# Performance work log

Measured on AMD Instinct MI355X. Metric: run time of the kernel, lower is better.

The kernel has to match this reference:

```python
import jax, jax.numpy as jnp
import numpy as np
from jax import lax

WINDOW_SIZE = 11
SIGMA = 1.5
C1 = 0.01 ** 2
C2 = 0.03 ** 2


def _gaussian_window(channels: int) -> jnp.ndarray:
    x = np.arange(WINDOW_SIZE)
    g = np.exp(-((x - WINDOW_SIZE // 2) ** 2) / (2.0 * SIGMA ** 2))
    g = g / g.sum()
    w2d = np.outer(g, g).astype(np.float32)  # [k,k]
    # depthwise kernel: [C, 1, k, k] in OIHW with feature_group_count=C
    return jnp.asarray(np.tile(w2d[None, None], (channels, 1, 1, 1)))


def _depthwise_blur(x: jnp.ndarray, window: jnp.ndarray) -> jnp.ndarray:
    pad = WINDOW_SIZE // 2
    return lax.conv_general_dilated(
        x, window,
        window_strides=(1, 1),
        padding=[(pad, pad), (pad, pad)],
        feature_group_count=x.shape[1],
        dimension_numbers=("NCHW", "OIHW", "NCHW"),
    )


def setup_inputs() -> dict:
    key = jax.random.key(0)
    k1, k2 = jax.random.split(key)
    pred = jax.random.normal(k1, (16, 3, 512, 512), dtype=jnp.float32)
    target = jax.random.normal(k2, (16, 3, 512, 512), dtype=jnp.float32)
    return {"pred": pred, "target": target}


def reference(pred, target):
    pred = (pred + 1.0) / 2.0
    target = (target + 1.0) / 2.0
    channels = pred.shape[1]
    window = _gaussian_window(channels)

    mu_p = _depthwise_blur(pred, window)
    mu_t = _depthwise_blur(target, window)
    mu_p_sq = mu_p * mu_p
    mu_t_sq = mu_t * mu_t
    mu_pt = mu_p * mu_t

    sigma_p_sq = _depthwise_blur(pred * pred, window) - mu_p_sq
    sigma_t_sq = _depthwise_blur(target * target, window) - mu_t_sq
    sigma_pt = _depthwise_blur(pred * target, window) - mu_pt

    ssim_map = ((2.0 * mu_pt + C1) * (2.0 * sigma_pt + C2)) / (
        (mu_p_sq + mu_t_sq + C1) * (sigma_p_sq + sigma_t_sq + C2)
    )
    return 1.0 - jnp.mean(ssim_map)
```

## Files before the change

### kernel.cpp

```cpp
#include <hip/hip_runtime.h>
#include <math.h>


#define IMG 512
#define TW 64
#define TH 16
#define GXD 8
#define GYD 32
#define GZD 48
#define NB (GXD * GYD * GZD)
#define VBS 88
#define C1c 0.0001f
#define C2c 0.0009f
#define NTOTAL 12582912.0f

typedef short bf16x8 __attribute__((ext_vector_type(8)));
typedef float f32x4 __attribute__((ext_vector_type(4)));
typedef float f32x2 __attribute__((ext_vector_type(2)));

struct GaussB { unsigned short gb[11]; };

__device__ __forceinline__ unsigned int pkbf(float a, float b) {
    return __builtin_amdgcn_perm(__float_as_uint(b), __float_as_uint(a),
                                 0x07060302u);
}

template <bool USE_ATOMIC>
__global__ __launch_bounds__(320, 6) void ssim_main(
    const float* __restrict__ pred,
    const float* __restrict__ target,
    float* __restrict__ sink,
    GaussB gwb)
{
    __shared__ unsigned short Wmat[16][32];
    __shared__ unsigned short vb[5][16][VBS];
    __shared__ float red[5];

    const int tid  = threadIdx.x;
    const int w    = tid >> 6;
    const int lane = tid & 63;
    const int quad = lane >> 4;
    const int n16  = lane & 15;
    const int tx0  = blockIdx.x * TW;
    const int ty0  = blockIdx.y * TH;
    const float* __restrict__ pbase = pred   + (size_t)blockIdx.z * (IMG * IMG);
    const float* __restrict__ tbase = target + (size_t)blockIdx.z * (IMG * IMG);

    for (int idx = tid; idx < 512; idx += 320) {
        int i = idx >> 5, k = idx & 31, d = k - i;
        Wmat[i][k] = (d >= 0 && d <= 10) ? gwb.gb[d] : 0;
    }
    __syncthreads();
    const bf16x8 wfrag = *(const bf16x8*)&Wmat[n16][quad * 8];

    const int gx   = tx0 - 5 + 16 * w + n16;
    const bool xin = (unsigned)gx < (unsigned)IMG;
    const int k0   = quad * 8;
    const int gy0  = ty0 - 5 + k0;
    const int vcol = 16 * w + 4 * quad;
    const f32x4 z = {0.0f, 0.0f, 0.0f, 0.0f};

    float pv[8], tv[8];
    {
        const bool ok = xin & (gy0 >= 0) & (gy0 <= IMG - 8);
        if (ok) {
            const float* pp = pbase + gy0 * IMG + gx;
            const float* tp = tbase + gy0 * IMG + gx;
            #pragma unroll
            for (int j = 0; j < 8; ++j) {
                pv[j] = pp[j * IMG];
                tv[j] = tp[j * IMG];
            }
        } else {
            #pragma unroll
            for (int j = 0; j < 8; ++j) {
                int gy = gy0 + j;
                bool in = xin && ((unsigned)gy < (unsigned)IMG);
                int idx = in ? (gy * IMG + gx) : 0;
                float a = pbase[idx];
                float b = tbase[idx];
                pv[j] = in ? a : 0.0f;
                tv[j] = in ? b : 0.0f;
            }
        }
    }

    const f32x2 halfv = {0.5f, 0.5f};
    f32x2 p2[4], t2[4];
    #pragma unroll
    for (int h = 0; h < 4; ++h) {
        f32x2 pr = {pv[2*h], pv[2*h+1]};
        f32x2 tr = {tv[2*h], tv[2*h+1]};
        p2[h] = pr * halfv + halfv;
        t2[h] = tr * halfv + halfv;
    }
    #pragma unroll
    for (int ch = 0; ch < 5; ++ch) {
        union { bf16x8 v; unsigned int u[4]; } f;
        #pragma unroll
        for (int h = 0; h < 4; ++h) {
            f32x2 q;
            if      (ch == 0) q = p2[h];
            else if (ch == 1) q = t2[h];
            else if (ch == 2) q = p2[h] * p2[h];
            else if (ch == 3) q = t2[h] * t2[h];
            else              q = p2[h] * t2[h];
            f.u[h] = pkbf(q.x, q.y);
        }
        f32x4 d = __builtin_amdgcn_mfma_f32_16x16x32_bf16(f.v, wfrag, z, 0, 0, 0);
        union { ushort4 s; unsigned int u[2]; } pk;
        pk.u[0] = pkbf(d[0], d[1]);
        pk.u[1] = pkbf(d[2], d[3]);
        *(ushort4*)&vb[ch][n16][vcol] = pk.s;
    }
    __syncthreads();

    float lsum = 0.0f;
    if (w < 4) {
        f32x4 r[5];
        #pragma unroll
        for (int ch = 0; ch < 5; ++ch) {
            bf16x8 a = *(const bf16x8*)&vb[ch][n16][16 * w + 8 * quad];
            r[ch] = __builtin_amdgcn_mfma_f32_16x16x32_bf16(a, wfrag, z, 0, 0, 0);
        }
        const f32x2 twov = {2.0f, 2.0f};
        const f32x2 c1v  = {C1c, C1c};
        const f32x2 c2v  = {C2c, C2c};
        #pragma unroll
        for (int jj = 0; jj < 2; ++jj) {
            f32x2 mp  = {r[0][2*jj], r[0][2*jj+1]};
            f32x2 mt  = {r[1][2*jj], r[1][2*jj+1]};
            f32x2 epp = {r[2][2*jj], r[2][2*jj+1]};
            f32x2 ett = {r[3][2*jj], r[3][2*jj+1]};
            f32x2 ept = {r[4][2*jj], r[4][2*jj+1]};
            f32x2 mp2 = mp * mp;
            f32x2 mt2 = mt * mt;
            f32x2 mpt = mp * mt;
            f32x2 sp_ = epp - mp2;
            f32x2 st_ = ett - mt2;
            f32x2 spt = ept - mpt;
            f32x2 num = (mpt * twov + c1v) * (spt * twov + c2v);
            f32x2 den = (mp2 + mt2 + c1v) * (sp_ + st_ + c2v);
            lsum = fmaf(num.x, __builtin_amdgcn_rcpf(den.x), lsum);
            lsum = fmaf(num.y, __builtin_amdgcn_rcpf(den.y), lsum);
        }
    }

    #pragma unroll
    for (int off = 32; off > 0; off >>= 1)
        lsum += __shfl_down(lsum, off, 64);
    if (lane == 0) red[w] = lsum;
    __syncthreads();
    if (tid == 0) {
        float s = red[0] + red[1] + red[2] + red[3];
        if (USE_ATOMIC) {
            atomicAdd(sink, s);
        } else {
            int bid = blockIdx.x + GXD * (blockIdx.y + GYD * blockIdx.z);
            sink[bid] = s;
        }
    }
}

__global__ __launch_bounds__(256) void ssim_reduce(const float* __restrict__ partials,
                                                   float* __restrict__ out)
{
    __shared__ float red[4];
    const int tid = threadIdx.x;
    float s = 0.0f;
    const float4* p4 = (const float4*)partials;
    #pragma unroll
    for (int j = 0; j < NB / 1024; ++j) {
        float4 v = p4[tid + 256 * j];
        s += v.x + v.y + v.z + v.w;
    }
    #pragma unroll
    for (int off = 32; off > 0; off >>= 1)
        s += __shfl_down(s, off, 64);
    if ((tid & 63) == 0) red[tid >> 6] = s;
    __syncthreads();
    if (tid == 0)
        out[0] = 1.0f - (red[0] + red[1] + red[2] + red[3]) / NTOTAL;
}

__global__ void ssim_zero(float* accum) { accum[0] = 0.0f; }
__global__ void ssim_final(const float* accum, float* out) {
    out[0] = 1.0f - accum[0] / NTOTAL;
}

extern "C" void kernel_launch(void* const* d_in, const int* in_sizes, int n_in,
                              void* d_out, int out_size, void* d_ws, size_t ws_size,
                              hipStream_t stream) {
    const float* pred   = (const float*)d_in[0];
    const float* target = (const float*)d_in[1];
    float* out = (float*)d_out;

    GaussB gwb;
    double vals[11], s = 0.0;
    for (int i = 0; i < 11; ++i) {
        double d = (double)i - 5.0;
        vals[i] = exp(-(d * d) / (2.0 * 1.5 * 1.5));
        s += vals[i];
    }
    for (int i = 0; i < 11; ++i) {
        float f = (float)(vals[i] / s);
        unsigned int u;
        __builtin_memcpy(&u, &f, 4);
        unsigned int rounded = (u + 0x7FFFu + ((u >> 16) & 1u)) >> 16;
        gwb.gb[i] = (unsigned short)rounded;
    }

    dim3 grid(GXD, GYD, GZD);
    if (ws_size >= (size_t)NB * sizeof(float)) {
        float* partials = (float*)d_ws;
        ssim_main<false><<<grid, 320, 0, stream>>>(pred, target, partials, gwb);
        ssim_reduce<<<1, 256, 0, stream>>>(partials, out);
    } else {
        float* accum = (float*)d_ws;
        ssim_zero<<<1, 1, 0, stream>>>(accum);
        ssim_main<true><<<grid, 320, 0, stream>>>(pred, target, accum, gwb);
        ssim_final<<<1, 1, 0, stream>>>(accum, out);
    }
}
```

Measured before the change: 136.3 us.

## Process eight row tiles per block with double-buffered register prefetch

Each block now walks 8 vertical tiles instead of one, so the grid shrinks to 4 blocks in y. The next tile's global loads are issued into a second register set before the horizontal pass of the current tile, which hides load latency. It also spreads the Gaussian matrix setup and block launch cost over more work. In exchange there are fewer blocks (1536) to fill the GPU, more registers in use, and the 10-row halo is still reloaded for every tile. The reduce loop was generalised to handle the smaller partial count.

```diff
diff --git a/kernel.cpp b/kernel.cpp
--- a/kernel.cpp
+++ b/kernel.cpp
@@ -5,8 +5,9 @@
 #define IMG 512
 #define TW 64
 #define TH 16
+#define YPB 8
 #define GXD 8
-#define GYD 32
+#define GYD 4
 #define GZD 48
 #define NB (GXD * GYD * GZD)
 #define VBS 88
@@ -42,26 +43,22 @@
     const int quad = lane >> 4;
     const int n16  = lane & 15;
     const int tx0  = blockIdx.x * TW;
-    const int ty0  = blockIdx.y * TH;
+    const int tyb  = blockIdx.y * (TH * YPB);
     const float* __restrict__ pbase = pred   + (size_t)blockIdx.z * (IMG * IMG);
     const float* __restrict__ tbase = target + (size_t)blockIdx.z * (IMG * IMG);
-
-    for (int idx = tid; idx < 512; idx += 320) {
-        int i = idx >> 5, k = idx & 31, d = k - i;
-        Wmat[i][k] = (d >= 0 && d <= 10) ? gwb.gb[d] : 0;
-    }
-    __syncthreads();
-    const bf16x8 wfrag = *(const bf16x8*)&Wmat[n16][quad * 8];
 
     const int gx   = tx0 - 5 + 16 * w + n16;
     const bool xin = (unsigned)gx < (unsigned)IMG;
     const int k0   = quad * 8;
-    const int gy0  = ty0 - 5 + k0;
     const int vcol = 16 * w + 4 * quad;
     const f32x4 z = {0.0f, 0.0f, 0.0f, 0.0f};
 
-    float pv[8], tv[8];
-    {
+    float pvA[8], tvA[8], pvB[8], tvB[8];
+    float lsum = 0.0f;
+    bf16x8 wfrag;
+
+    auto load_tile = [&](int it, float (&pv)[8], float (&tv)[8]) {
+        const int gy0 = tyb + it * TH - 5 + k0;
         const bool ok = xin & (gy0 >= 0) & (gy0 <= IMG - 8);
         if (ok) {
             const float* pp = pbase + gy0 * IMG + gx;
@@ -83,67 +80,93 @@
                 tv[j] = in ? b : 0.0f;
             }
         }
-    }
-
-    const f32x2 halfv = {0.5f, 0.5f};
-    f32x2 p2[4], t2[4];
-    #pragma unroll
-    for (int h = 0; h < 4; ++h) {
-        f32x2 pr = {pv[2*h], pv[2*h+1]};
-        f32x2 tr = {tv[2*h], tv[2*h+1]};
-        p2[h] = pr * halfv + halfv;
-        t2[h] = tr * halfv + halfv;
-    }
-    #pragma unroll
-    for (int ch = 0; ch < 5; ++ch) {
-        union { bf16x8 v; unsigned int u[4]; } f;
+    };
+
+    load_tile(0, pvA, tvA);
+
+    for (int idx = tid; idx < 512; idx += 320) {
+        int i = idx >> 5, k = idx & 31, d = k - i;
+        Wmat[i][k] = (d >= 0 && d <= 10) ? gwb.gb[d] : 0;
+    }
+    __syncthreads();
+    wfrag = *(const bf16x8*)&Wmat[n16][quad * 8];
+
+    auto pass_v = [&](const float (&pv)[8], const float (&tv)[8]) {
+        const f32x2 halfv = {0.5f, 0.5f};
+        f32x2 p2[4], t2[4];
         #pragma unroll
         for (int h = 0; h < 4; ++h) {
-            f32x2 q;
-            if      (ch == 0) q = p2[h];
-            else if (ch == 1) q = t2[h];
-            else if (ch == 2) q = p2[h] * p2[h];
-            else if (ch == 3) q = t2[h] * t2[h];
-            else              q = p2[h] * t2[h];
-            f.u[h] = pkbf(q.x, q.y);
-        }
-        f32x4 d = __builtin_amdgcn_mfma_f32_16x16x32_bf16(f.v, wfrag, z, 0, 0, 0);
-        union { ushort4 s; unsigned int u[2]; } pk;
-        pk.u[0] = pkbf(d[0], d[1]);
-        pk.u[1] = pkbf(d[2], d[3]);
-        *(ushort4*)&vb[ch][n16][vcol] = pk.s;
-    }
-    __syncthreads();
-
-    float lsum = 0.0f;
-    if (w < 4) {
-        f32x4 r[5];
+            f32x2 pr = {pv[2*h], pv[2*h+1]};
+            f32x2 tr = {tv[2*h], tv[2*h+1]};
+            p2[h] = pr * halfv + halfv;
+            t2[h] = tr * halfv + halfv;
+        }
         #pragma unroll
         for (int ch = 0; ch < 5; ++ch) {
-            bf16x8 a = *(const bf16x8*)&vb[ch][n16][16 * w + 8 * quad];
-            r[ch] = __builtin_amdgcn_mfma_f32_16x16x32_bf16(a, wfrag, z, 0, 0, 0);
-        }
-        const f32x2 twov = {2.0f, 2.0f};
-        const f32x2 c1v  = {C1c, C1c};
-        const f32x2 c2v  = {C2c, C2c};
-        #pragma unroll
-        for (int jj = 0; jj < 2; ++jj) {
-            f32x2 mp  = {r[0][2*jj], r[0][2*jj+1]};
-            f32x2 mt  = {r[1][2*jj], r[1][2*jj+1]};
-            f32x2 epp = {r[2][2*jj], r[2][2*jj+1]};
-            f32x2 ett = {r[3][2*jj], r[3][2*jj+1]};
-            f32x2 ept = {r[4][2*jj], r[4][2*jj+1]};
-            f32x2 mp2 = mp * mp;
-            f32x2 mt2 = mt * mt;
-            f32x2 mpt = mp * mt;
-            f32x2 sp_ = epp - mp2;
-            f32x2 st_ = ett - mt2;
-            f32x2 spt = ept - mpt;
-            f32x2 num = (mpt * twov + c1v) * (spt * twov + c2v);
-            f32x2 den = (mp2 + mt2 + c1v) * (sp_ + st_ + c2v);
-            lsum = fmaf(num.x, __builtin_amdgcn_rcpf(den.x), lsum);
-            lsum = fmaf(num.y, __builtin_amdgcn_rcpf(den.y), lsum);
-        }
+            union { bf16x8 v; unsigned int u[4]; } f;
+            #pragma unroll
+            for (int h = 0; h < 4; ++h) {
+                f32x2 q;
+                if      (ch == 0) q = p2[h];
+                else if (ch == 1) q = t2[h];
+                else if (ch == 2) q = p2[h] * p2[h];
+                else if (ch == 3) q = t2[h] * t2[h];
+                else              q = p2[h] * t2[h];
+                f.u[h] = pkbf(q.x, q.y);
+            }
+            f32x4 d = __builtin_amdgcn_mfma_f32_16x16x32_bf16(f.v, wfrag, z, 0, 0, 0);
+            union { ushort4 s; unsigned int u[2]; } pk;
+            pk.u[0] = pkbf(d[0], d[1]);
+            pk.u[1] = pkbf(d[2], d[3]);
+            *(ushort4*)&vb[ch][n16][vcol] = pk.s;
+        }
+    };
+
+    auto pass_h = [&]() {
+        if (w < 4) {
+            f32x4 r[5];
+            #pragma unroll
+            for (int ch = 0; ch < 5; ++ch) {
+                bf16x8 a = *(const bf16x8*)&vb[ch][n16][16 * w + 8 * quad];
+                r[ch] = __builtin_amdgcn_mfma_f32_16x16x32_bf16(a, wfrag, z, 0, 0, 0);
+            }
+            const f32x2 twov = {2.0f, 2.0f};
+            const f32x2 c1v  = {C1c, C1c};
+            const f32x2 c2v  = {C2c, C2c};
+            #pragma unroll
+            for (int jj = 0; jj < 2; ++jj) {
+                f32x2 mp  = {r[0][2*jj], r[0][2*jj+1]};
+                f32x2 mt  = {r[1][2*jj], r[1][2*jj+1]};
+                f32x2 epp = {r[2][2*jj], r[2][2*jj+1]};
+                f32x2 ett = {r[3][2*jj], r[3][2*jj+1]};
+                f32x2 ept = {r[4][2*jj], r[4][2*jj+1]};
+                f32x2 mp2 = mp * mp;
+                f32x2 mt2 = mt * mt;
+                f32x2 mpt = mp * mt;
+                f32x2 sp_ = epp - mp2;
+                f32x2 st_ = ett - mt2;
+                f32x2 spt = ept - mpt;
+                f32x2 num = (mpt * twov + c1v) * (spt * twov + c2v);
+                f32x2 den = (mp2 + mt2 + c1v) * (sp_ + st_ + c2v);
+                lsum = fmaf(num.x, __builtin_amdgcn_rcpf(den.x), lsum);
+                lsum = fmaf(num.y, __builtin_amdgcn_rcpf(den.y), lsum);
+            }
+        }
+    };
+
+    #pragma unroll 1
+    for (int it2 = 0; it2 < YPB; it2 += 2) {
+        pass_v(pvA, tvA);
+        __syncthreads();
+        load_tile(it2 + 1, pvB, tvB);
+        pass_h();
+        __syncthreads();
+
+        pass_v(pvB, tvB);
+        __syncthreads();
+        if (it2 + 2 < YPB) load_tile(it2 + 2, pvA, tvA);
+        pass_h();
+        __syncthreads();
     }
 
     #pragma unroll
@@ -169,9 +192,8 @@
     const int tid = threadIdx.x;
     float s = 0.0f;
     const float4* p4 = (const float4*)partials;
-    #pragma unroll
-    for (int j = 0; j < NB / 1024; ++j) {
-        float4 v = p4[tid + 256 * j];
+    for (int j = tid; j < NB / 4; j += 256) {
+        float4 v = p4[j];
         s += v.x + v.y + v.z + v.w;
     }
     #pragma unroll
```

Result: slower. 150.0 us (+10.1%).
